# Kernel optimization log

Hardware: AMD Instinct MI355X
Metric: run time of the kernel (lower is better)

Reference implementation:

```python
import jax, jax.numpy as jnp
import numpy as np

B, N, D = 8, 512, 1024
E, H, TOP_K = 8, 8, 2
HD = D // H
EPS = 1e-5


def setup_inputs() -> dict:
    key = jax.random.key(0)
    ks = jax.random.split(key, 8)
    # kaiming_uniform with a=sqrt(5) over fan_in=N -> bound = sqrt(6/((1+5)*N)) = 1/sqrt(N)
    bound_w = 1.0 / np.sqrt(N)
    bound_lin = 1.0 / np.sqrt(D)
    return {
        "x": jax.random.normal(ks[0], (B, N, D), dtype=jnp.float32),
        "weight": jax.random.uniform(ks[1], (E, H, N, N), jnp.float32, -bound_w, bound_w),
        "bias": jnp.zeros((E, H, N), jnp.float32),
        "router_w": jax.random.uniform(ks[2], (E, D), jnp.float32, -bound_lin, bound_lin),
        "in_w": jax.random.uniform(ks[3], (D, D), jnp.float32, -bound_lin, bound_lin),
        "in_b": jax.random.uniform(ks[4], (D,), jnp.float32, -bound_lin, bound_lin),
        "out_w": jax.random.uniform(ks[5], (D, D), jnp.float32, -bound_lin, bound_lin),
        "out_b": jax.random.uniform(ks[6], (D,), jnp.float32, -bound_lin, bound_lin),
    }


def reference(x, weight, bias, router_w, in_w, in_b, out_w, out_b):
    # Router: mean-pool tokens, linear, softmax, top-k
    router_logits = x.mean(axis=1) @ router_w.T              # (B, E)
    router_probs = jax.nn.softmax(router_logits, axis=-1)
    top_w, top_i = jax.lax.top_k(router_probs, TOP_K)        # (B, K)
    top_w = top_w / top_w.sum(axis=-1, keepdims=True)

    # Input projection -> (B, H, hd, N), layer-norm over token axis N (no affine)
    xp = x @ in_w.T + in_b                                   # (B, N, D)
    xr = xp.reshape(B, N, H, HD).transpose(0, 2, 3, 1)       # (B, H, hd, N)
    mu = xr.mean(axis=-1, keepdims=True)
    var = xr.var(axis=-1, keepdims=True)
    xn = (xr - mu) * jax.lax.rsqrt(var + EPS)

    # Gather per-(batch, head, k) NxN expert matrices, row-softmax
    w = weight[top_i].transpose(0, 2, 1, 3, 4)               # (B, H, K, N, N)
    b = bias[top_i].transpose(0, 2, 1, 3)                    # (B, H, K, N)
    w_attn = jax.nn.softmax(w, axis=-1)

    # out[b,h,k,d,m] = sum_n xn[b,h,d,n] * w_attn[b,h,k,m,n]
    out = jnp.einsum('bhdn,bhkmn->bhkdm', xn, w_attn)
    out = out + b[:, :, :, None, :]                          # (B, H, K, hd, N)
    out = (out * top_w[:, None, :, None, None]).sum(axis=2)  # (B, H, hd, N)

    out = out.transpose(0, 3, 1, 2).reshape(B, N, D)         # (B, N, D)
    out = out @ out_w.T + out_b

    # Load-balancing aux loss
    top1 = top_i[:, 0]
    expert_mask = jax.nn.one_hot(top1, E, dtype=jnp.float32)
    aux = E * (router_probs.mean(axis=0) * expert_mask.mean(axis=0)).sum()
    return out, aux
```

## Files before the change

kernel.cpp:

```cpp
#include <hip/hip_runtime.h>
#include <hip/hip_bf16.h>

#define Bv 8
#define Nv 512
#define Dv 1024
#define Ev 8
#define Hv 8
#define HDv 128
#define EPSv 1e-5f

typedef __attribute__((ext_vector_type(8))) short short8;
typedef __attribute__((ext_vector_type(4))) float f32x4;

__device__ __forceinline__ unsigned short f2b(float f) {
    __hip_bfloat16 h = __float2bfloat16(f);
    return *reinterpret_cast<unsigned short*>(&h);
}
__device__ __forceinline__ float bf2f(unsigned int u) {
    union { unsigned int i; float f; } v; v.i = u << 16; return v.f;
}
__device__ __forceinline__ unsigned int blend2(unsigned int a, unsigned int b,
                                               float tw0, float tw1) {
    float lo = tw0 * bf2f(a & 0xffffu) + tw1 * bf2f(b & 0xffffu);
    float hi = tw0 * bf2f(a >> 16)     + tw1 * bf2f(b >> 16);
    return (unsigned int)f2b(lo) | ((unsigned int)f2b(hi) << 16);
}

__device__ __forceinline__ void gld16(const void* g, void* l) {
    __builtin_amdgcn_global_load_lds(
        (const __attribute__((address_space(1))) void*)(uintptr_t)(g),
        (__attribute__((address_space(3))) void*)(uintptr_t)(l), 16, 0, 0);
}

__global__ __launch_bounds__(256) void k_pre(const float* __restrict__ x,
                                             const float* __restrict__ weight,
                                             const float* __restrict__ w1,
                                             const float* __restrict__ w2,
                                             unsigned short* __restrict__ xb,
                                             float* __restrict__ part_x,
                                             unsigned short* __restrict__ wa,
                                             unsigned short* __restrict__ w1b,
                                             unsigned short* __restrict__ w2b) {
    int bid = blockIdx.x;
    int t = threadIdx.x;
    if (bid < 128) {
        int b = bid >> 4, c = bid & 15;
        const float* px = x + ((size_t)b * Nv + c * 32) * Dv + t * 4;
        unsigned short* qx = xb + ((size_t)b * Nv + c * 32) * Dv + t * 4;
        float4 s4 = make_float4(0.f, 0.f, 0.f, 0.f);
        #pragma unroll 8
        for (int r = 0; r < 32; ++r) {
            float4 v = *(const float4*)(px + (size_t)r * Dv);
            s4.x += v.x; s4.y += v.y; s4.z += v.z; s4.w += v.w;
            uint2 pk;
            pk.x = (unsigned)f2b(v.x) | ((unsigned)f2b(v.y) << 16);
            pk.y = (unsigned)f2b(v.z) | ((unsigned)f2b(v.w) << 16);
            *(uint2*)(qx + (size_t)r * Dv) = pk;
        }
        *(float4*)(part_x + ((size_t)(b * 16 + c)) * Dv + t * 4) = s4;
        return;
    }
    if (bid < 128 + 8192) {
        int wave = (bid - 128) * 4 + (t >> 6);
        int lane = t & 63;
        const float* row = weight + (size_t)wave * Nv;
        const float4* r4 = (const float4*)(row + lane * 8);
        float4 a = r4[0], b = r4[1];
        float v[8] = {a.x, a.y, a.z, a.w, b.x, b.y, b.z, b.w};
        float mx = v[0];
        #pragma unroll
        for (int i = 1; i < 8; ++i) mx = fmaxf(mx, v[i]);
        for (int off = 1; off < 64; off <<= 1) mx = fmaxf(mx, __shfl_xor(mx, off));
        float s = 0.f;
        #pragma unroll
        for (int i = 0; i < 8; ++i) { v[i] = __expf(v[i] - mx); s += v[i]; }
        for (int off = 1; off < 64; off <<= 1) s += __shfl_xor(s, off);
        float inv = 1.f / s;
        union { unsigned short h[8]; uint4 u; } pk;
        #pragma unroll
        for (int i = 0; i < 8; ++i) pk.h[i] = f2b(v[i] * inv);
        *(uint4*)(wa + (size_t)wave * Nv + lane * 8) = pk.u;
        return;
    }
    int c = (bid - 8320) * 256 + t;
    const float* src; unsigned short* dst; int off;
    if (c < 131072) { src = w1; dst = w1b; off = c; }
    else            { src = w2; dst = w2b; off = c - 131072; }
    float4 a = ((const float4*)src)[off * 2];
    float4 b = ((const float4*)src)[off * 2 + 1];
    union { unsigned short h[8]; uint4 u; } pk;
    pk.h[0] = f2b(a.x); pk.h[1] = f2b(a.y); pk.h[2] = f2b(a.z); pk.h[3] = f2b(a.w);
    pk.h[4] = f2b(b.x); pk.h[5] = f2b(b.y); pk.h[6] = f2b(b.z); pk.h[7] = f2b(b.w);
    ((uint4*)dst)[off] = pk.u;
}

template <int MODE>
__global__ __launch_bounds__(256) void k_gemm(
    const unsigned short* __restrict__ A,
    const unsigned short* __restrict__ W,
    const float* __restrict__ bias,
    void* __restrict__ Cv,
    float2* __restrict__ part,
    const float* __restrict__ part_x,
    float* __restrict__ xmean,
    int M, int Nn, int K) {
    __shared__ __align__(16) unsigned short sA[3][128 * 64];
    __shared__ __align__(16) unsigned short sB[3][128 * 64];
    const int t = threadIdx.x;
    const int bn = blockIdx.x * 128;
    const int bm = blockIdx.y * 128;
    const int lane = t & 63;
    const int w = t >> 6, wm = w >> 1, wn = w & 1;
    const int fr = lane & 15, fq = lane >> 4;
    const int NT = K >> 6;
    f32x4 acc[4][4] = {};

#define STAGE(s, k0)                                                        \
    {                                                                       \
        _Pragma("unroll")                                                   \
        for (int i_ = 0; i_ < 4; ++i_) {                                    \
            int c_ = t + i_ * 256;                                          \
            int row_ = c_ >> 3, col_ = c_ & 7;                              \
            int cs_ = col_ ^ (row_ & 7);                                    \
            gld16(A + (size_t)(bm + row_) * K + (k0) + cs_ * 8, &sA[s][c_ * 8]); \
            gld16(W + (size_t)(bn + row_) * K + (k0) + cs_ * 8, &sB[s][c_ * 8]); \
        }                                                                   \
    }

    STAGE(0, 0);
    STAGE(1, 64);
    if (MODE == 2) {
        int blk = blockIdx.y * 8 + blockIdx.x;
        int o = blk * 32 + (t >> 3);
        int c2 = t & 7;
        int b2 = o >> 10, d2 = o & 1023;
        float S = part_x[((size_t)(b2 * 16 + c2)) * Dv + d2]
                + part_x[((size_t)(b2 * 16 + c2 + 8)) * Dv + d2];
        S += __shfl_xor(S, 1); S += __shfl_xor(S, 2); S += __shfl_xor(S, 4);
        if (c2 == 0) xmean[o] = S * (1.f / Nv);
    }
    for (int it = 0; it < NT; ++it) {
        if (it + 2 < NT) {
            STAGE((it + 2) % 3, (it + 2) * 64);
            asm volatile("s_waitcnt vmcnt(16)" ::: "memory");
        } else if (it + 1 < NT) {
            asm volatile("s_waitcnt vmcnt(8)" ::: "memory");
        } else {
            asm volatile("s_waitcnt vmcnt(0)" ::: "memory");
        }
        __builtin_amdgcn_s_barrier();
        const unsigned short* pA = sA[it % 3];
        const unsigned short* pB = sB[it % 3];
        #pragma unroll
        for (int kk = 0; kk < 2; ++kk) {
            short8 af[4], bv[4];
            #pragma unroll
            for (int i = 0; i < 4; ++i)
                af[i] = *(const short8*)&pA[(wm * 64 + i * 16 + fr) * 64 + (((kk << 2) + fq) ^ (fr & 7)) * 8];
            #pragma unroll
            for (int j = 0; j < 4; ++j)
                bv[j] = *(const short8*)&pB[(wn * 64 + j * 16 + fr) * 64 + (((kk << 2) + fq) ^ (fr & 7)) * 8];
            #pragma unroll
            for (int i = 0; i < 4; ++i)
                #pragma unroll
                for (int j = 0; j < 4; ++j)
                    acc[i][j] = __builtin_amdgcn_mfma_f32_16x16x32_bf16(af[i], bv[j], acc[i][j], 0, 0, 0);
        }
        __builtin_amdgcn_s_barrier();
    }
#undef STAGE
    if (MODE == 0) {
        #pragma unroll
        for (int j = 0; j < 4; ++j) {
            const int n = bn + wn * 64 + j * 16 + fr;
            const float bj = bias[n];
            #pragma unroll
            for (int i = 0; i < 4; ++i) {
                const int m0 = bm + wm * 64 + i * 16 + fq * 4;
                #pragma unroll
                for (int r = 0; r < 4; ++r)
                    ((float*)Cv)[(size_t)(m0 + r) * Nn + n] = acc[i][j][r] + bj;
            }
        }
    } else {
        unsigned short* sc = &sA[0][0];
        float2* red = (float2*)&sB[0][0];
        const int bB   = bm >> 9;
        const int tok0 = bm & 511;
        const int chunk = (bm >> 7) & 3;
        #pragma unroll
        for (int j = 0; j < 4; ++j) {
            const int col = wn * 64 + j * 16 + fr;
            const float bj = bias[bn + col];
            float s = 0.f, q = 0.f;
            #pragma unroll
            for (int i = 0; i < 4; ++i) {
                const int row0 = wm * 64 + i * 16 + fq * 4;
                #pragma unroll
                for (int r = 0; r < 4; r += 2) {
                    float v0 = acc[i][j][r] + bj;
                    float v1 = acc[i][j][r + 1] + bj;
                    s += v0 + v1;
                    q = fmaf(v0, v0, fmaf(v1, v1, q));
                    unsigned int pk = (unsigned int)f2b(v0) | ((unsigned int)f2b(v1) << 16);
                    *(unsigned int*)&sc[col * 136 + row0 + r] = pk;
                }
            }
            red[col * 8 + wm * 4 + fq] = make_float2(s, q);
        }
        __syncthreads();
        if (t < 128) {
            float S = 0.f, Q = 0.f;
            #pragma unroll
            for (int k = 0; k < 8; ++k) { float2 v = red[t * 8 + k]; S += v.x; Q += v.y; }
            part[((size_t)bB * Dv + bn + t) * 4 + chunk] = make_float2(S, Q);
        }
        unsigned short* dst = (unsigned short*)Cv;
        #pragma unroll
        for (int k = 0; k < 8; ++k) {
            const int c = t + k * 256;
            const int dl = c >> 4, tk = c & 15;
            uint4 v = *(const uint4*)&sc[dl * 136 + tk * 8];
            *(uint4*)&dst[((size_t)bB * Dv + bn + dl) * Nv + tok0 + tk * 8] = v;
        }
    }
}

__global__ __launch_bounds__(256) void k_mixg(
    const unsigned short* __restrict__ wa,
    const unsigned short* __restrict__ xpT,
    const float* __restrict__ bias,
    const float* __restrict__ xmean,
    const float* __restrict__ router_w,
    const float2* __restrict__ part,
    unsigned short* __restrict__ y,
    float* __restrict__ aux_out) {
    __shared__ __align__(16) unsigned short sA[2][128 * 64];
    __shared__ __align__(16) unsigned short sB[2][128 * 64];
    __shared__ float probs[Bv][Ev];
    __shared__ float twsh[Bv][2];
    __shared__ int   tsel[Bv][2];
    __shared__ int   top1s[Bv];
    const int t = threadIdx.x;
    const int bm = blockIdx.x * 128;
    const int bh = blockIdx.y;
    const int b = bh >> 3, h = bh & 7;

    {
        int pid = t >> 2, l = t & 3;
        int rb = pid >> 3, re = pid & 7;
        const float4* xm = (const float4*)(xmean + rb * Dv);
        const float4* rw = (const float4*)(router_w + re * Dv);
        float s = 0.f;
        #pragma unroll
        for (int j = 0; j < 64; ++j) {
            float4 aa = xm[l + j * 4], ww = rw[l + j * 4];
            s = fmaf(aa.x, ww.x, s); s = fmaf(aa.y, ww.y, s);
            s = fmaf(aa.z, ww.z, s); s = fmaf(aa.w, ww.w, s);
        }
        s += __shfl_xor(s, 1); s += __shfl_xor(s, 2);
        if (l == 0) probs[rb][re] = s;
    }
    __syncthreads();
    if (t < Bv) {
        int bb = t;
        float mx = -1e30f;
        for (int e2 = 0; e2 < Ev; ++e2) mx = fmaxf(mx, probs[bb][e2]);
        float sum = 0.f;
        for (int e2 = 0; e2 < Ev; ++e2) { float v = __expf(probs[bb][e2] - mx); probs[bb][e2] = v; sum += v; }
        float inv = 1.f / sum;
        for (int e2 = 0; e2 < Ev; ++e2) probs[bb][e2] *= inv;
        int i0 = 0; float p0 = probs[bb][0];
        for (int e2 = 1; e2 < Ev; ++e2) if (probs[bb][e2] > p0) { p0 = probs[bb][e2]; i0 = e2; }
        int i1 = -1; float p1 = -1.f;
        for (int e2 = 0; e2 < Ev; ++e2) if (e2 != i0 && probs[bb][e2] > p1) { p1 = probs[bb][e2]; i1 = e2; }
        float s2 = p0 + p1;
        tsel[bb][0] = i0; tsel[bb][1] = i1;
        twsh[bb][0] = p0 / s2; twsh[bb][1] = p1 / s2;
        top1s[bb] = i0;
    }
    __syncthreads();
    if (blockIdx.x == 0 && bh == 0 && t == 0) {
        float aux = 0.f;
        for (int e2 = 0; e2 < Ev; ++e2) {
            float pm = 0.f, mm = 0.f;
            for (int bb = 0; bb < Bv; ++bb) { pm += probs[bb][e2]; mm += (top1s[bb] == e2) ? 1.f : 0.f; }
            aux += (pm / Bv) * (mm / Bv);
        }
        *aux_out = aux * Ev;
    }
    const int e0 = tsel[b][0], e1 = tsel[b][1];
    const float tw0 = twsh[b][0], tw1 = twsh[b][1];

    const int lane = t & 63;
    const int w = t >> 6, wm = w >> 1, wn = w & 1;
    const int fr = lane & 15, fq = lane >> 4;

    float rstd_j[4], nmr_j[4];
    #pragma unroll
    for (int j = 0; j < 4; ++j) {
        const int dg = h * HDv + wn * 64 + j * 16 + fr;
        const float2* pp = part + ((size_t)b * Dv + dg) * 4;
        float S = 0.f, Q = 0.f;
        #pragma unroll
        for (int cc = 0; cc < 4; ++cc) { float2 v = pp[cc]; S += v.x; Q += v.y; }
        float mu = S * (1.f / Nv);
        float var = Q * (1.f / Nv) - mu * mu;
        float rs = rsqrtf(var + EPSv);
        rstd_j[j] = rs; nmr_j[j] = -mu * rs;
    }

    const unsigned short* A0 = wa + (size_t)(e0 * Hv + h) * Nv * Nv;
    const unsigned short* A1 = wa + (size_t)(e1 * Hv + h) * Nv * Nv;
    const unsigned short* Bb = xpT + ((size_t)b * Dv + h * HDv) * Nv;
    const int NT = Nv >> 6;
    f32x4 acc[4][4] = {};
    uint4 ra0[4], ra1[4];

#define BSTAGE(s, k0)                                                       \
    {                                                                       \
        _Pragma("unroll")                                                   \
        for (int i_ = 0; i_ < 4; ++i_) {                                    \
            int c_ = t + i_ * 256;                                          \
            int row_ = c_ >> 3, col_ = c_ & 7;                              \
            int cs_ = col_ ^ (row_ & 7);                                    \
            gld16(Bb + (size_t)row_ * Nv + (k0) + cs_ * 8, &sB[s][c_ * 8]); \
        }                                                                   \
    }
#define ALOAD(k0)                                                           \
    {                                                                       \
        _Pragma("unroll")                                                   \
        for (int i_ = 0; i_ < 4; ++i_) {                                    \
            int c_ = t + i_ * 256;                                          \
            int row_ = c_ >> 3, col_ = c_ & 7;                              \
            int cs_ = col_ ^ (row_ & 7);                                    \
            size_t off_ = (size_t)(bm + row_) * Nv + (k0) + cs_ * 8;        \
            ra0[i_] = *(const uint4*)&A0[off_];                             \
            ra1[i_] = *(const uint4*)&A1[off_];                             \
        }                                                                   \
    }

    BSTAGE(0, 0);
    ALOAD(0);
    for (int it = 0; it < NT; ++it) {
        if (it + 1 < NT) {
            BSTAGE((it + 1) & 1, (it + 1) * 64);
            asm volatile("s_waitcnt vmcnt(4)" ::: "memory");
        } else {
            asm volatile("s_waitcnt vmcnt(0)" ::: "memory");
        }
        #pragma unroll
        for (int i = 0; i < 4; ++i) {
            int c = t + i * 256;
            uint4 o;
            o.x = blend2(ra0[i].x, ra1[i].x, tw0, tw1);
            o.y = blend2(ra0[i].y, ra1[i].y, tw0, tw1);
            o.z = blend2(ra0[i].z, ra1[i].z, tw0, tw1);
            o.w = blend2(ra0[i].w, ra1[i].w, tw0, tw1);
            *(uint4*)&sA[it & 1][c * 8] = o;
        }
        if (it + 1 < NT) ALOAD((it + 1) * 64);
        asm volatile("s_waitcnt lgkmcnt(0)" ::: "memory");
        __builtin_amdgcn_s_barrier();
        const unsigned short* pA = sA[it & 1];
        const unsigned short* pB = sB[it & 1];
        #pragma unroll
        for (int kk = 0; kk < 2; ++kk) {
            short8 af[4], bv[4];
            #pragma unroll
            for (int i = 0; i < 4; ++i)
                af[i] = *(const short8*)&pA[(wm * 64 + i * 16 + fr) * 64 + (((kk << 2) + fq) ^ (fr & 7)) * 8];
            #pragma unroll
            for (int j = 0; j < 4; ++j)
                bv[j] = *(const short8*)&pB[(wn * 64 + j * 16 + fr) * 64 + (((kk << 2) + fq) ^ (fr & 7)) * 8];
            #pragma unroll
            for (int i = 0; i < 4; ++i)
                #pragma unroll
                for (int j = 0; j < 4; ++j)
                    acc[i][j] = __builtin_amdgcn_mfma_f32_16x16x32_bf16(af[i], bv[j], acc[i][j], 0, 0, 0);
        }
        __builtin_amdgcn_s_barrier();
    }
#undef BSTAGE
#undef ALOAD
    #pragma unroll
    for (int i = 0; i < 4; ++i) {
        #pragma unroll
        for (int r = 0; r < 4; ++r) {
            const int m = bm + wm * 64 + i * 16 + fq * 4 + r;
            const float br = tw0 * bias[(size_t)(e0 * Hv + h) * Nv + m]
                           + tw1 * bias[(size_t)(e1 * Hv + h) * Nv + m];
            #pragma unroll
            for (int j = 0; j < 4; ++j) {
                const int d = wn * 64 + j * 16 + fr;
                float v = fmaf(acc[i][j][r], rstd_j[j], nmr_j[j] + br);
                y[((size_t)b * Nv + m) * Dv + h * HDv + d] = f2b(v);
            }
        }
    }
}

extern "C" void kernel_launch(void* const* d_in, const int* in_sizes, int n_in,
                              void* d_out, int out_size, void* d_ws, size_t ws_size,
                              hipStream_t stream) {
    const float* x        = (const float*)d_in[0];
    const float* weight   = (const float*)d_in[1];
    const float* bias     = (const float*)d_in[2];
    const float* router_w = (const float*)d_in[3];
    const float* in_w     = (const float*)d_in[4];
    const float* in_b     = (const float*)d_in[5];
    const float* out_w    = (const float*)d_in[6];
    const float* out_b    = (const float*)d_in[7];
    float* out = (float*)d_out;

    if (ws_size < ((size_t)63 << 20)) return;

    char* wsb = (char*)d_ws;
    float*  xmean  = (float*)(wsb);
    float2* part   = (float2*)(wsb + 65536);
    float*  part_x = (float*)(wsb + 327680);
    unsigned short* in_wb  = (unsigned short*)(wsb + ((size_t)1 << 20));
    unsigned short* out_wb = (unsigned short*)(wsb + ((size_t)3 << 20));
    unsigned short* xb     = (unsigned short*)(wsb + ((size_t)5 << 20));
    unsigned short* xpT    = (unsigned short*)(wsb + ((size_t)13 << 20));
    unsigned short* wa     = (unsigned short*)(wsb + ((size_t)29 << 20));
    unsigned short* y = xb;

    k_pre<<<9344, 256, 0, stream>>>(x, weight, in_w, out_w, xb, part_x, wa, in_wb, out_wb);
    k_gemm<2><<<dim3(8, 32), 256, 0, stream>>>(xb, in_wb, in_b, xpT, part, part_x, xmean,
                                               Bv * Nv, Dv, Dv);
    k_mixg<<<dim3(4, 64), 256, 0, stream>>>(wa, xpT, bias, xmean, router_w, part, y,
                                            out + (size_t)Bv * Nv * Dv);
    k_gemm<0><<<dim3(8, 32), 256, 0, stream>>>(y, out_wb, out_b, out, nullptr, nullptr, nullptr,
                                               Bv * Nv, Dv, Dv);
}
```

Before: 74.87 us.

## Fuse expert softmax into mixing GEMM using precomputed row max and sum stats

The pre-kernel no longer writes a full bf16 softmaxed copy of all expert weight matrices. It computes only per-row max and inverse sum. The mixing kernel now reads fp32 weights directly and applies exp, normalization and top-k blending while staging into shared memory. This removes a large bf16 write and re-read of the whole weight tensor, at the cost of fp32 loads (twice the bytes per element) and extra exp work inside the GEMM's A-staging loop.

Result: slower. 76.93 us (+2.8%).

```diff
diff --git a/kernel.cpp b/kernel.cpp
--- a/kernel.cpp
+++ b/kernel.cpp
@@ -19,12 +19,6 @@
 __device__ __forceinline__ float bf2f(unsigned int u) {
     union { unsigned int i; float f; } v; v.i = u << 16; return v.f;
 }
-__device__ __forceinline__ unsigned int blend2(unsigned int a, unsigned int b,
-                                               float tw0, float tw1) {
-    float lo = tw0 * bf2f(a & 0xffffu) + tw1 * bf2f(b & 0xffffu);
-    float hi = tw0 * bf2f(a >> 16)     + tw1 * bf2f(b >> 16);
-    return (unsigned int)f2b(lo) | ((unsigned int)f2b(hi) << 16);
-}
 
 __device__ __forceinline__ void gld16(const void* g, void* l) {
     __builtin_amdgcn_global_load_lds(
@@ -38,13 +32,54 @@
                                              const float* __restrict__ w2,
                                              unsigned short* __restrict__ xb,
                                              float* __restrict__ part_x,
-                                             unsigned short* __restrict__ wa,
+                                             float2* __restrict__ rstat,
                                              unsigned short* __restrict__ w1b,
                                              unsigned short* __restrict__ w2b) {
     int bid = blockIdx.x;
     int t = threadIdx.x;
-    if (bid < 128) {
-        int b = bid >> 4, c = bid & 15;
+    if (bid < 2048) {
+        int lane = t & 63;
+        int r0 = bid * 16 + (t >> 6) * 4;
+        const float* wp = weight + (size_t)r0 * Nv + lane * 8;
+        float4 va[4][2];
+        #pragma unroll
+        for (int r = 0; r < 4; ++r) {
+            va[r][0] = *(const float4*)(wp + (size_t)r * Nv);
+            va[r][1] = *(const float4*)(wp + (size_t)r * Nv + 4);
+        }
+        float mx[4], sm[4];
+        #pragma unroll
+        for (int r = 0; r < 4; ++r) {
+            float4 a = va[r][0], b = va[r][1];
+            mx[r] = fmaxf(fmaxf(fmaxf(a.x, a.y), fmaxf(a.z, a.w)),
+                          fmaxf(fmaxf(b.x, b.y), fmaxf(b.z, b.w)));
+        }
+        for (int off = 1; off < 64; off <<= 1) {
+            #pragma unroll
+            for (int r = 0; r < 4; ++r) mx[r] = fmaxf(mx[r], __shfl_xor(mx[r], off));
+        }
+        #pragma unroll
+        for (int r = 0; r < 4; ++r) {
+            float4 a = va[r][0], b = va[r][1];
+            sm[r] = __expf(a.x - mx[r]) + __expf(a.y - mx[r])
+                  + __expf(a.z - mx[r]) + __expf(a.w - mx[r])
+                  + __expf(b.x - mx[r]) + __expf(b.y - mx[r])
+                  + __expf(b.z - mx[r]) + __expf(b.w - mx[r]);
+        }
+        for (int off = 1; off < 64; off <<= 1) {
+            #pragma unroll
+            for (int r = 0; r < 4; ++r) sm[r] += __shfl_xor(sm[r], off);
+        }
+        if (lane == 0) {
+            #pragma unroll
+            for (int r = 0; r < 4; ++r)
+                rstat[r0 + r] = make_float2(mx[r], 1.f / sm[r]);
+        }
+        return;
+    }
+    if (bid < 2048 + 128) {
+        int xb2 = bid - 2048;
+        int b = xb2 >> 4, c = xb2 & 15;
         const float* px = x + ((size_t)b * Nv + c * 32) * Dv + t * 4;
         unsigned short* qx = xb + ((size_t)b * Nv + c * 32) * Dv + t * 4;
         float4 s4 = make_float4(0.f, 0.f, 0.f, 0.f);
@@ -60,29 +95,7 @@
         *(float4*)(part_x + ((size_t)(b * 16 + c)) * Dv + t * 4) = s4;
         return;
     }
-    if (bid < 128 + 8192) {
-        int wave = (bid - 128) * 4 + (t >> 6);
-        int lane = t & 63;
-        const float* row = weight + (size_t)wave * Nv;
-        const float4* r4 = (const float4*)(row + lane * 8);
-        float4 a = r4[0], b = r4[1];
-        float v[8] = {a.x, a.y, a.z, a.w, b.x, b.y, b.z, b.w};
-        float mx = v[0];
-        #pragma unroll
-        for (int i = 1; i < 8; ++i) mx = fmaxf(mx, v[i]);
-        for (int off = 1; off < 64; off <<= 1) mx = fmaxf(mx, __shfl_xor(mx, off));
-        float s = 0.f;
-        #pragma unroll
-        for (int i = 0; i < 8; ++i) { v[i] = __expf(v[i] - mx); s += v[i]; }
-        for (int off = 1; off < 64; off <<= 1) s += __shfl_xor(s, off);
-        float inv = 1.f / s;
-        union { unsigned short h[8]; uint4 u; } pk;
-        #pragma unroll
-        for (int i = 0; i < 8; ++i) pk.h[i] = f2b(v[i] * inv);
-        *(uint4*)(wa + (size_t)wave * Nv + lane * 8) = pk.u;
-        return;
-    }
-    int c = (bid - 8320) * 256 + t;
+    int c = (bid - 2176) * 256 + t;
     const float* src; unsigned short* dst; int off;
     if (c < 131072) { src = w1; dst = w1b; off = c; }
     else            { src = w2; dst = w2b; off = c - 131072; }
@@ -227,7 +240,8 @@
 }
 
 __global__ __launch_bounds__(256) void k_mixg(
-    const unsigned short* __restrict__ wa,
+    const float* __restrict__ weight,
+    const float2* __restrict__ rstat,
     const unsigned short* __restrict__ xpT,
     const float* __restrict__ bias,
     const float* __restrict__ xmean,
@@ -310,12 +324,24 @@
         rstd_j[j] = rs; nmr_j[j] = -mu * rs;
     }
 
-    const unsigned short* A0 = wa + (size_t)(e0 * Hv + h) * Nv * Nv;
-    const unsigned short* A1 = wa + (size_t)(e1 * Hv + h) * Nv * Nv;
+    const float* W0 = weight + (size_t)(e0 * Hv + h) * Nv * Nv;
+    const float* W1 = weight + (size_t)(e1 * Hv + h) * Nv * Nv;
+    const float2* R0 = rstat + (size_t)(e0 * Hv + h) * Nv;
+    const float2* R1 = rstat + (size_t)(e1 * Hv + h) * Nv;
     const unsigned short* Bb = xpT + ((size_t)b * Dv + h * HDv) * Nv;
+
+    float m0s[4], c0s[4], m1s[4], c1s[4];
+    #pragma unroll
+    for (int i = 0; i < 4; ++i) {
+        int rg = bm + (t >> 3) + i * 32;
+        float2 s0 = R0[rg], s1 = R1[rg];
+        m0s[i] = s0.x; c0s[i] = tw0 * s0.y;
+        m1s[i] = s1.x; c1s[i] = tw1 * s1.y;
+    }
+
     const int NT = Nv >> 6;
     f32x4 acc[4][4] = {};
-    uint4 ra0[4], ra1[4];
+    float4 ra0[4][2], ra1[4][2];
 
 #define BSTAGE(s, k0)                                                       \
     {                                                                       \
@@ -335,8 +361,10 @@
             int row_ = c_ >> 3, col_ = c_ & 7;                              \
             int cs_ = col_ ^ (row_ & 7);                                    \
             size_t off_ = (size_t)(bm + row_) * Nv + (k0) + cs_ * 8;        \
-            ra0[i_] = *(const uint4*)&A0[off_];                             \
-            ra1[i_] = *(const uint4*)&A1[off_];                             \
+            ra0[i_][0] = *(const float4*)&W0[off_];                         \
+            ra0[i_][1] = *(const float4*)&W0[off_ + 4];                     \
+            ra1[i_][0] = *(const float4*)&W1[off_];                         \
+            ra1[i_][1] = *(const float4*)&W1[off_ + 4];                     \
         }                                                                   \
     }
 
@@ -352,12 +380,23 @@
         #pragma unroll
         for (int i = 0; i < 4; ++i) {
             int c = t + i * 256;
-            uint4 o;
-            o.x = blend2(ra0[i].x, ra1[i].x, tw0, tw1);
-            o.y = blend2(ra0[i].y, ra1[i].y, tw0, tw1);
-            o.z = blend2(ra0[i].z, ra1[i].z, tw0, tw1);
-            o.w = blend2(ra0[i].w, ra1[i].w, tw0, tw1);
-            *(uint4*)&sA[it & 1][c * 8] = o;
+            float o[8];
+            const float4 a0 = ra0[i][0], a1 = ra0[i][1];
+            const float4 b0 = ra1[i][0], b1 = ra1[i][1];
+            o[0] = c0s[i] * __expf(a0.x - m0s[i]) + c1s[i] * __expf(b0.x - m1s[i]);
+            o[1] = c0s[i] * __expf(a0.y - m0s[i]) + c1s[i] * __expf(b0.y - m1s[i]);
+            o[2] = c0s[i] * __expf(a0.z - m0s[i]) + c1s[i] * __expf(b0.z - m1s[i]);
+            o[3] = c0s[i] * __expf(a0.w - m0s[i]) + c1s[i] * __expf(b0.w - m1s[i]);
+            o[4] = c0s[i] * __expf(a1.x - m0s[i]) + c1s[i] * __expf(b1.x - m1s[i]);
+            o[5] = c0s[i] * __expf(a1.y - m0s[i]) + c1s[i] * __expf(b1.y - m1s[i]);
+            o[6] = c0s[i] * __expf(a1.z - m0s[i]) + c1s[i] * __expf(b1.z - m1s[i]);
+            o[7] = c0s[i] * __expf(a1.w - m0s[i]) + c1s[i] * __expf(b1.w - m1s[i]);
+            uint4 pk;
+            pk.x = (unsigned)f2b(o[0]) | ((unsigned)f2b(o[1]) << 16);
+            pk.y = (unsigned)f2b(o[2]) | ((unsigned)f2b(o[3]) << 16);
+            pk.z = (unsigned)f2b(o[4]) | ((unsigned)f2b(o[5]) << 16);
+            pk.w = (unsigned)f2b(o[6]) | ((unsigned)f2b(o[7]) << 16);
+            *(uint4*)&sA[it & 1][c * 8] = pk;
         }
         if (it + 1 < NT) ALOAD((it + 1) * 64);
         asm volatile("s_waitcnt lgkmcnt(0)" ::: "memory");
@@ -417,19 +456,19 @@
 
     char* wsb = (char*)d_ws;
     float*  xmean  = (float*)(wsb);
-    float2* part   = (float2*)(wsb + 65536);
-    float*  part_x = (float*)(wsb + 327680);
-    unsigned short* in_wb  = (unsigned short*)(wsb + ((size_t)1 << 20));
-    unsigned short* out_wb = (unsigned short*)(wsb + ((size_t)3 << 20));
-    unsigned short* xb     = (unsigned short*)(wsb + ((size_t)5 << 20));
-    unsigned short* xpT    = (unsigned short*)(wsb + ((size_t)13 << 20));
-    unsigned short* wa     = (unsigned short*)(wsb + ((size_t)29 << 20));
+    float2* part   = (float2*)(wsb + (64 << 10));
+    float*  part_x = (float*)(wsb + (512 << 10));
+    float2* rstat  = (float2*)(wsb + ((size_t)1 << 20));
+    unsigned short* in_wb  = (unsigned short*)(wsb + ((size_t)2 << 20));
+    unsigned short* out_wb = (unsigned short*)(wsb + ((size_t)4 << 20));
+    unsigned short* xb     = (unsigned short*)(wsb + ((size_t)8 << 20));
+    unsigned short* xpT    = (unsigned short*)(wsb + ((size_t)16 << 20));
     unsigned short* y = xb;
 
-    k_pre<<<9344, 256, 0, stream>>>(x, weight, in_w, out_w, xb, part_x, wa, in_wb, out_wb);
+    k_pre<<<3200, 256, 0, stream>>>(x, weight, in_w, out_w, xb, part_x, rstat, in_wb, out_wb);
     k_gemm<2><<<dim3(8, 32), 256, 0, stream>>>(xb, in_wb, in_b, xpT, part, part_x, xmean,
                                                Bv * Nv, Dv, Dv);
-    k_mixg<<<dim3(4, 64), 256, 0, stream>>>(wa, xpT, bias, xmean, router_w, part, y,
+    k_mixg<<<dim3(4, 64), 256, 0, stream>>>(weight, rstat, xpT, bias, xmean, router_w, part, y,
                                             out + (size_t)Bv * Nv * Dv);
     k_gemm<0><<<dim3(8, 32), 256, 0, stream>>>(y, out_wb, out_b, out, nullptr, nullptr, nullptr,
                                                Bv * Nv, Dv, Dv);
```
